# Optimization experiments

Hardware: AMD Instinct MI355X
Metric: run time of the kernel (lower is better)

The kernel has to match this reference:

```python
import jax, jax.numpy as jnp
import numpy as np

B = 4194304
K_HIGH_PRESSURE = 0.0244
I_THRESH = 0.39063

DIFFPRESS_KP = jnp.array([-10., -2.5, -1., 1., 2.5, 10.], jnp.float32)
PID_KP = jnp.array([0.5, 0.3417968, 0.3417968, 0.3417968, 0.3417968, 0.5], jnp.float32)
DIFFPRESS_KI = jnp.array([-10., -2.5, -1., 1., 2.5, 10.], jnp.float32)
PID_KI = jnp.array([0.1503906]*6, jnp.float32)
LO_PRESS = jnp.array([100., 150, 200, 250, 300, 350, 400, 450, 500, 550], jnp.float32)
HI_PRESS = jnp.array([200., 400, 600, 800, 1000, 1200, 1400, 1600, 1800, 2000], jnp.float32)
COM_SPEED_MIN = jnp.array([
 [2000.,2000,2000,2000,2000,2000,2000,2000,2000,2000],
 [1600,1600,1600,1600,1600,1700,1800,1900,2000,2000],
 [1200,1200,1200,1200,1200,1200,1200,1200,1600,2000],
 [900,900,950,1000,1050,1100,1150,1200,1600,2000],
 [800,800,800,800,900,1000,1100,1200,1600,2000],
 [800,800,800,800,800,900,1050,1200,1600,2000],
 [800,800,800,800,800,800,1000,1200,1600,2000],
 [800,800,800,800,800,800,950,1200,1600,2000],
 [800,800,800,800,800,800,900,1200,1600,2000],
 [800,800,800,800,800,800,850,1200,1600,2000]], jnp.float32)


def _interp1d(xp, fp, x):
    # linear interp with edge clamping, same as torch-style inter1D
    return jnp.interp(x, xp, fp)


def _interp2d(xp, yp, z, x, y):
    # bilinear interpolation over z[xi, yi], edges clamped
    xi = jnp.clip(jnp.searchsorted(xp, x) - 1, 0, xp.shape[0] - 2)
    yi = jnp.clip(jnp.searchsorted(yp, y) - 1, 0, yp.shape[0] - 2)
    x0, x1 = xp[xi], xp[xi + 1]
    y0, y1 = yp[yi], yp[yi + 1]
    tx = jnp.clip((x - x0) / (x1 - x0), 0.0, 1.0)
    ty = jnp.clip((y - y0) / (y1 - y0), 0.0, 1.0)
    z00 = z[xi, yi]; z01 = z[xi, yi + 1]; z10 = z[xi + 1, yi]; z11 = z[xi + 1, yi + 1]
    return (z00 * (1 - tx) * (1 - ty) + z10 * tx * (1 - ty)
            + z01 * (1 - tx) * ty + z11 * tx * ty)


def setup_inputs() -> dict:
    key = jax.random.key(0)
    ks = jax.random.split(key, 8)
    x = jax.random.normal(ks[0], (B, 13), jnp.float32)
    # make pressure-ish columns plausible positive values
    x = x.at[:, 4].set(jnp.abs(x[:, 4]) * 100.0 + 200.0)   # lo_pressure
    x = x.at[:, 5].set(jnp.abs(x[:, 5]) * 300.0 + 1000.0)  # hi_pressure
    x = x.at[:, 7].set(jnp.abs(x[:, 7]) * 300.0 + 1000.0)  # aim_hi_pressure
    last = jax.random.normal(ks[1], (B, 1), jnp.float32)
    xavier = lambda k, fi, fo: jax.random.uniform(k, (fi, fo), jnp.float32,
                                                  -np.sqrt(6.0/(fi+fo)), np.sqrt(6.0/(fi+fo)))
    return {
        "x": x,
        "last_ac_pid_out_hp": last,
        "k_w1": xavier(ks[2], 1, 8), "k_b1": jnp.zeros((8,), jnp.float32),
        "k_w2": xavier(ks[3], 8, 8), "k_b2": jnp.zeros((8,), jnp.float32),
        "k_w3": xavier(ks[4], 8, 1), "k_b3": jnp.zeros((1,), jnp.float32),
    }


def reference(x, last_ac_pid_out_hp, k_w1, k_b1, k_w2, k_b2, k_w3, k_b3):
    lo_pressure = x[:, 4]
    hi_pressure = x[:, 5]
    aim_hi_pressure = x[:, 7]
    ac_kp_rate_last = x[:, 11]

    diff_hp = (aim_hi_pressure - hi_pressure) * K_HIGH_PRESSURE        # [B]
    # parameters_k MLP: 1 -> 8 -> 8 -> 1, tanh activations
    h = jnp.tanh(diff_hp[:, None] @ k_w1 + k_b1)
    h = jnp.tanh(h @ k_w2 + k_b2)
    k_out = h @ k_w3 + k_b3                                            # [B,1]
    diff_hp_real = (aim_hi_pressure - hi_pressure)[:, None] * k_out    # [B,1]

    ac_kp_rate = jax.lax.stop_gradient(ac_kp_rate_last)
    Kp = _interp1d(DIFFPRESS_KP, PID_KP, diff_hp) * ac_kp_rate         # [B]
    Ki = _interp1d(DIFFPRESS_KI, PID_KI, diff_hp) * ac_kp_rate         # [B]

    com_speed_min = _interp2d(LO_PRESS, HI_PRESS, COM_SPEED_MIN,
                              lo_pressure, hi_pressure)  # computed, unused (as in source)
    del com_speed_min

    # I-term update; initial Ivalue / last_Pout / last_Dout are zeros
    ivalue = jnp.where(jnp.abs(diff_hp[:, None]) < I_THRESH,
                       jnp.zeros_like(diff_hp_real),
                       diff_hp_real * 0.5)
    Iout = Ki[:, None] * ivalue          # last_Ivalue = 0
    Pout = Kp[:, None] * diff_hp_real
    Diffout = Pout                        # Dout = 0, last_Pout = last_Dout = 0
    offset = Iout + Diffout
    return last_ac_pid_out_hp + offset    # [B,1]
```

## Files before the change

### kernel.cpp

```cpp
#include <hip/hip_runtime.h>

#define K_HP 0.0244f
#define I_THRESH 0.39063f

__device__ __forceinline__ float tanh_fast(float v) {
    float e = __expf(2.0f * v);
    float r = __builtin_amdgcn_rcpf(1.0f + e);
    return fmaf(-2.0f, r, 1.0f);
}

__global__ __launch_bounds__(256) void pid_kernel(
    const float* __restrict__ x,
    const float* __restrict__ last,
    const float* __restrict__ w1, const float* __restrict__ b1,
    const float* __restrict__ w2, const float* __restrict__ b2,
    const float* __restrict__ w3, const float* __restrict__ b3,
    float* __restrict__ out, int n)
{
    float W1[8], B1[8], W2[64], B2[8], W3[8];
    #pragma unroll
    for (int j = 0; j < 8; ++j) { W1[j] = w1[j]; B1[j] = b1[j]; B2[j] = b2[j]; W3[j] = w3[j]; }
    #pragma unroll
    for (int j = 0; j < 64; ++j) W2[j] = w2[j];
    const float B3 = b3[0];

    const float a   = 0.3417968f;
    const float Kic = 0.1503906f;

    int idx    = blockIdx.x * blockDim.x + threadIdx.x;
    int stride = gridDim.x * blockDim.x;
    for (int i = idx; i < n; i += stride) {
        const float* row = x + (size_t)i * 13;
        float hi   = row[5];
        float aim  = row[7];
        float rate = row[11];

        float d_raw = aim - hi;
        float diff  = d_raw * K_HP;

        float h1[8];
        #pragma unroll
        for (int j = 0; j < 8; ++j) h1[j] = tanh_fast(fmaf(diff, W1[j], B1[j]));
        float k_out = B3;
        #pragma unroll
        for (int j = 0; j < 8; ++j) {
            float acc = B2[j];
            #pragma unroll
            for (int k = 0; k < 8; ++k) acc = fmaf(h1[k], W2[k * 8 + j], acc);
            k_out = fmaf(tanh_fast(acc), W3[j], k_out);
        }
        float diff_real = d_raw * k_out;

        float ad = fabsf(diff);
        float t  = fminf(fmaxf((ad - 2.5f) * (1.0f / 7.5f), 0.0f), 1.0f);
        float Kp = fmaf(t, 0.5f - a, a) * rate;
        float Ki = Kic * rate;

        float ivalue = (ad < I_THRESH) ? 0.0f : diff_real * 0.5f;
        out[i] = last[i] + fmaf(Ki, ivalue, Kp * diff_real);
    }
}

extern "C" void kernel_launch(void* const* d_in, const int* in_sizes, int n_in,
                              void* d_out, int out_size, void* d_ws, size_t ws_size,
                              hipStream_t stream) {
    const float* x    = (const float*)d_in[0];
    const float* last = (const float*)d_in[1];
    const float* w1   = (const float*)d_in[2];
    const float* b1   = (const float*)d_in[3];
    const float* w2   = (const float*)d_in[4];
    const float* b2   = (const float*)d_in[5];
    const float* w3   = (const float*)d_in[6];
    const float* b3   = (const float*)d_in[7];
    float* out = (float*)d_out;
    int n = out_size;
    pid_kernel<<<2048, 256, 0, stream>>>(x, last, w1, b1, w2, b2, w3, b3, out, n);
}
```

Baseline: 46.71 us.

## Stage row tiles through LDS with coalesced float4 loads

Each block now loads a 256-row tile of the 13-column input into shared memory using coalesced float4 reads, then each thread reads its three needed columns from LDS. This replaces strided per-thread scalar loads. The grid size is also raised to up to 4096 blocks. The cost is two block barriers per tile and no overlap of loading with compute within a block. All input columns are loaded even though only three are used.

```diff
diff --git a/kernel.cpp b/kernel.cpp
--- a/kernel.cpp
+++ b/kernel.cpp
@@ -9,6 +9,9 @@
     return fmaf(-2.0f, r, 1.0f);
 }
 
+constexpr int ROWS = 256;
+constexpr int TILE_F4 = ROWS * 13 / 4;
+
 __global__ __launch_bounds__(256) void pid_kernel(
     const float* __restrict__ x,
     const float* __restrict__ last,
@@ -17,6 +20,9 @@
     const float* __restrict__ w3, const float* __restrict__ b3,
     float* __restrict__ out, int n)
 {
+    __shared__ float4 lds4[TILE_F4];
+    float* lds = (float*)lds4;
+
     float W1[8], B1[8], W2[64], B2[8], W3[8];
     #pragma unroll
     for (int j = 0; j < 8; ++j) { W1[j] = w1[j]; B1[j] = b1[j]; B2[j] = b2[j]; W3[j] = w3[j]; }
@@ -27,37 +33,54 @@
     const float a   = 0.3417968f;
     const float Kic = 0.1503906f;
 
-    int idx    = blockIdx.x * blockDim.x + threadIdx.x;
-    int stride = gridDim.x * blockDim.x;
-    for (int i = idx; i < n; i += stride) {
-        const float* row = x + (size_t)i * 13;
-        float hi   = row[5];
-        float aim  = row[7];
-        float rate = row[11];
+    const int t = threadIdx.x;
+    const int nTiles = (n + ROWS - 1) / ROWS;
 
-        float d_raw = aim - hi;
-        float diff  = d_raw * K_HP;
+    for (int tile = blockIdx.x; tile < nTiles; tile += gridDim.x) {
+        const size_t base = (size_t)tile * ROWS * 13;
+        const int rowsHere = min(ROWS, n - tile * ROWS);
 
-        float h1[8];
-        #pragma unroll
-        for (int j = 0; j < 8; ++j) h1[j] = tanh_fast(fmaf(diff, W1[j], B1[j]));
-        float k_out = B3;
-        #pragma unroll
-        for (int j = 0; j < 8; ++j) {
-            float acc = B2[j];
+        if (rowsHere == ROWS) {
+            const float4* src = (const float4*)(x + base);
             #pragma unroll
-            for (int k = 0; k < 8; ++k) acc = fmaf(h1[k], W2[k * 8 + j], acc);
-            k_out = fmaf(tanh_fast(acc), W3[j], k_out);
+            for (int k = 0; k < 3; ++k) lds4[t + k * 256] = src[t + k * 256];
+            if (t < TILE_F4 - 768) lds4[t + 768] = src[t + 768];
+        } else {
+            for (int j = t; j < rowsHere * 13; j += 256) lds[j] = x[base + j];
         }
-        float diff_real = d_raw * k_out;
+        __syncthreads();
 
-        float ad = fabsf(diff);
-        float t  = fminf(fmaxf((ad - 2.5f) * (1.0f / 7.5f), 0.0f), 1.0f);
-        float Kp = fmaf(t, 0.5f - a, a) * rate;
-        float Ki = Kic * rate;
+        if (t < rowsHere) {
+            const int i = tile * ROWS + t;
+            float hi   = lds[t * 13 + 5];
+            float aim  = lds[t * 13 + 7];
+            float rate = lds[t * 13 + 11];
 
-        float ivalue = (ad < I_THRESH) ? 0.0f : diff_real * 0.5f;
-        out[i] = last[i] + fmaf(Ki, ivalue, Kp * diff_real);
+            float d_raw = aim - hi;
+            float diff  = d_raw * K_HP;
+
+            float h1[8];
+            #pragma unroll
+            for (int j = 0; j < 8; ++j) h1[j] = tanh_fast(fmaf(diff, W1[j], B1[j]));
+            float k_out = B3;
+            #pragma unroll
+            for (int j = 0; j < 8; ++j) {
+                float acc = B2[j];
+                #pragma unroll
+                for (int k = 0; k < 8; ++k) acc = fmaf(h1[k], W2[k * 8 + j], acc);
+                k_out = fmaf(tanh_fast(acc), W3[j], k_out);
+            }
+            float diff_real = d_raw * k_out;
+
+            float ad = fabsf(diff);
+            float tt = fminf(fmaxf((ad - 2.5f) * (1.0f / 7.5f), 0.0f), 1.0f);
+            float Kp = fmaf(tt, 0.5f - a, a) * rate;
+            float Ki = Kic * rate;
+
+            float ivalue = (ad < I_THRESH) ? 0.0f : diff_real * 0.5f;
+            out[i] = last[i] + fmaf(Ki, ivalue, Kp * diff_real);
+        }
+        __syncthreads();
     }
 }
 
@@ -74,5 +97,7 @@
     const float* b3   = (const float*)d_in[7];
     float* out = (float*)d_out;
     int n = out_size;
-    pid_kernel<<<2048, 256, 0, stream>>>(x, last, w1, b1, w2, b2, w3, b3, out, n);
+    int nTiles = (n + ROWS - 1) / ROWS;
+    int grid = nTiles < 4096 ? nTiles : 4096;
+    pid_kernel<<<grid, 256, 0, stream>>>(x, last, w1, b1, w2, b2, w3, b3, out, n);
 }
```

Result: slower. 49.49 us (+5.9%).
